# Kernel optimization log

Measured on AMD Instinct MI355X. Metric: run time of the kernel, lower is better.

## Reference

```python
import jax, jax.numpy as jnp
import numpy as np

HQ, HKV = 16, 4          # query heads, kv heads
ROPE_BASE = 10000.0


def _rope(t, positions):
    # t: [B, H, S, hd]; standard rotate-half RoPE over head_dim
    hd = t.shape[-1]
    inv_freq = 1.0 / (ROPE_BASE ** (jnp.arange(0, hd, 2, dtype=jnp.float32) / hd))
    freqs = positions.astype(jnp.float32)[:, None] * inv_freq[None, :]      # [S, hd/2]
    emb = jnp.concatenate([freqs, freqs], axis=-1)                           # [S, hd]
    cos = jnp.cos(emb)[None, None, :, :].astype(t.dtype)
    sin = jnp.sin(emb)[None, None, :, :].astype(t.dtype)
    t1, t2 = t[..., : hd // 2], t[..., hd // 2 :]
    rot = jnp.concatenate([-t2, t1], axis=-1)
    return t * cos + rot * sin


def setup_inputs() -> dict:
    key = jax.random.key(0)
    k0, k1, k2, k3, k4 = jax.random.split(key, 5)
    B, S, D = 2, 2048, 2048
    hd = D // HQ
    x = jax.random.normal(k0, (B, S, D), dtype=jnp.float32)
    s = 0.02
    wq = jax.random.normal(k1, (HQ * hd, D), dtype=jnp.float32) * s
    wk = jax.random.normal(k2, (HKV * hd, D), dtype=jnp.float32) * s
    wv = jax.random.normal(k3, (HKV * hd, D), dtype=jnp.float32) * s
    wo = jax.random.normal(k4, (D, HQ * hd), dtype=jnp.float32) * s
    return {"x": x, "wq": wq, "wk": wk, "wv": wv, "wo": wo}


def reference(x, wq, wk, wv, wo):
    B, S, D = x.shape
    hd = D // HQ
    G = HQ // HKV
    positions = jnp.arange(S)

    q = (x @ wq.T).reshape(B, S, HQ, hd).transpose(0, 2, 1, 3)   # [B,Hq,S,hd]
    k = (x @ wk.T).reshape(B, S, HKV, hd).transpose(0, 2, 1, 3)  # [B,Hkv,S,hd]
    v = (x @ wv.T).reshape(B, S, HKV, hd).transpose(0, 2, 1, 3)

    q = _rope(q, positions)
    k = _rope(k, positions)

    # GQA: expand KV heads to match query heads (repeat_interleave on head dim)
    k = jnp.repeat(k, G, axis=1)
    v = jnp.repeat(v, G, axis=1)

    scores = jnp.einsum("bhqd,bhkd->bhqk", q, k) / jnp.sqrt(jnp.float32(hd))
    causal = jnp.tril(jnp.ones((S, S), dtype=bool))
    scores = jnp.where(causal[None, None], scores, -jnp.inf)
    attn = jax.nn.softmax(scores, axis=-1)

    out = jnp.einsum("bhqk,bhkd->bhqd", attn, v)                 # [B,Hq,S,hd]
    out = out.transpose(0, 2, 1, 3).reshape(B, S, HQ * hd)
    return out @ wo.T
```

## Files before the change

kernel.cpp:

```cpp
#include <hip/hip_runtime.h>

#define B_   2
#define S_   2048
#define D_   2048
#define HQ_  16
#define HKV_ 4
#define HD_  128

typedef __attribute__((ext_vector_type(4))) float f32x4;
typedef __attribute__((ext_vector_type(16))) float f32x16;
typedef __attribute__((ext_vector_type(4))) short s16x4;
typedef __attribute__((ext_vector_type(8))) short s16x8;

static __device__ __forceinline__ ushort f2bf(float f) {
  uint32_t u = __float_as_uint(f);
  u += 0x7fffu + ((u >> 16) & 1u);
  return (ushort)(u >> 16);
}

static __device__ __forceinline__ void gload16(const ushort* g, ushort* l) {
  __builtin_amdgcn_global_load_lds((const __attribute__((address_space(1))) uint32_t*)(g),
                                   (__attribute__((address_space(3))) uint32_t*)(l), 16, 0, 0);
}

__global__ void cast_kernel(const float* __restrict__ in, ushort* __restrict__ out, int n) {
  int i = (blockIdx.x * blockDim.x + threadIdx.x) * 4;
  if (i + 3 < n) {
    float4 v = *(const float4*)(in + i);
    *(ushort4*)(out + i) = make_ushort4(f2bf(v.x), f2bf(v.y), f2bf(v.z), f2bf(v.w));
  }
}

__global__ __launch_bounds__(256) void gemm_nt_bf16(const ushort* __restrict__ A,
                                                    const ushort* __restrict__ Bm,
                                                    float* __restrict__ C,
                                                    int M, int N, int K, int nbx) {
  __shared__ ushort As[128 * 64];
  __shared__ ushort Bs[128 * 64];
  const int nwg = gridDim.x;
  const int per = nwg >> 3;
  const int id = blockIdx.x;
  const int wg = (id & 7) * per + (id >> 3);
  const int bx = wg % nbx, by = wg / nbx;
  const int tid  = threadIdx.x;
  const int lane = tid & 63;
  const int wave = tid >> 6;
  const int lrow = lane & 15, lgrp = lane >> 4;
  const int wm = (wave >> 1) * 64, wn = (wave & 1) * 64;
  const int brow = by * 128, bcol = bx * 128;

  f32x4 acc[4][4];
#pragma unroll
  for (int i = 0; i < 4; ++i)
#pragma unroll
    for (int j = 0; j < 4; ++j) acc[i][j] = (f32x4){0.f, 0.f, 0.f, 0.f};

  const int r_ = tid >> 3, c16 = tid & 7;
  const ushort* Abase = A + (size_t)brow * K;
  const ushort* Bbase = Bm + (size_t)bcol * K;

  for (int k0 = 0; k0 < K; k0 += 64) {
#pragma unroll
    for (int q = 0; q < 4; ++q) {
      const int row = q * 32 + r_;
      const int sc = c16 ^ (row & 7);
      gload16(Abase + (size_t)row * K + k0 + sc * 8, &As[q * 2048 + wave * 512]);
      gload16(Bbase + (size_t)row * K + k0 + sc * 8, &Bs[q * 2048 + wave * 512]);
    }
    __syncthreads();
#pragma unroll
    for (int kc = 0; kc < 2; ++kc) {
      s16x8 aF[4], bF[4];
#pragma unroll
      for (int mt = 0; mt < 4; ++mt) {
        const int row = wm + mt * 16 + lrow;
        aF[mt] = *(const s16x8*)&As[row * 64 + ((kc * 32 + lgrp * 8) ^ ((row & 7) << 3))];
      }
#pragma unroll
      for (int nt = 0; nt < 4; ++nt) {
        const int row = wn + nt * 16 + lrow;
        bF[nt] = *(const s16x8*)&Bs[row * 64 + ((kc * 32 + lgrp * 8) ^ ((row & 7) << 3))];
      }
#pragma unroll
      for (int mt = 0; mt < 4; ++mt)
#pragma unroll
        for (int nt = 0; nt < 4; ++nt)
          acc[mt][nt] = __builtin_amdgcn_mfma_f32_16x16x32_bf16(aF[mt], bF[nt], acc[mt][nt], 0, 0, 0);
    }
    __syncthreads();
  }
#pragma unroll
  for (int mt = 0; mt < 4; ++mt) {
#pragma unroll
    for (int nt = 0; nt < 4; ++nt) {
      const int row = brow + wm + mt * 16 + lgrp * 4;
      const int col = bcol + wn + nt * 16 + lrow;
#pragma unroll
      for (int rr = 0; rr < 4; ++rr)
        C[(size_t)(row + rr) * N + col] = acc[mt][nt][rr];
    }
  }
}

__global__ __launch_bounds__(256) void rope_qk(const float* __restrict__ qkv,
                                               ushort* __restrict__ Qb, ushort* __restrict__ Kb) {
  const int idx = blockIdx.x * 256 + threadIdx.x;
  const int i = idx & 63;
  const int t = idx >> 6;
  const int s = t & (S_ - 1);
  const int b = t >> 11;
  const float inv = exp2f(-(float)i * 0.20762050594046832f);
  float sn, cs;
  sincosf((float)s * inv, &sn, &cs);
  const size_t row = (size_t)t * 3072;
  const float SCL2 = 0.12751744716705736f;
#pragma unroll
  for (int h = 0; h < HQ_; ++h) {
    const float a  = qkv[row + h * 128 + i];
    const float c2 = qkv[row + h * 128 + i + 64];
    const size_t ob = ((size_t)((b * HQ_ + h) * S_ + s)) * 128;
    Qb[ob + i]      = f2bf((a * cs - c2 * sn) * SCL2);
    Qb[ob + i + 64] = f2bf((c2 * cs + a * sn) * SCL2);
  }
#pragma unroll
  for (int kh = 0; kh < HKV_; ++kh) {
    const float a  = qkv[row + 2048 + kh * 128 + i];
    const float c2 = qkv[row + 2048 + kh * 128 + i + 64];
    const size_t ob = ((size_t)((b * HKV_ + kh) * S_ + s)) * 128;
    Kb[ob + i]      = f2bf(a * cs - c2 * sn);
    Kb[ob + i + 64] = f2bf(c2 * cs + a * sn);
  }
}

__global__ __launch_bounds__(256) void v_transpose(const float* __restrict__ qkv, ushort* __restrict__ Vt) {
  __shared__ ushort tile[128][72];
  const int s0 = blockIdx.x * 64;
  const int kh = blockIdx.y;
  const int b  = blockIdx.z;
  for (int idx = threadIdx.x; idx < 64 * 128; idx += 256) {
    int sl = idx >> 7;
    int d  = idx & 127;
    float v = qkv[(size_t)(b * S_ + s0 + sl) * 3072 + 2560 + kh * 128 + d];
    tile[d][sl] = f2bf(v);
  }
  __syncthreads();
  for (int idx = threadIdx.x; idx < 64 * 128; idx += 256) {
    int d  = idx >> 6;
    int sl = idx & 63;
    int sp = (sl & 48) | (sl & 3) | ((sl & 8) >> 1) | ((sl & 4) << 1);
    Vt[((size_t)(b * HKV_ + kh) * 128 + d) * S_ + s0 + sp] = tile[d][sl];
  }
}

__global__ __launch_bounds__(256, 2) void attn_kernel(const ushort* __restrict__ Qb,
                                                      const ushort* __restrict__ Kb,
                                                      const ushort* __restrict__ Vt,
                                                      ushort* __restrict__ Ao) {
  __shared__ ushort Ks[2][64 * 128];
  __shared__ ushort Vs[2][128 * 64];
  const int h = blockIdx.y, b = blockIdx.z, kh = h >> 2;
  const int tid = threadIdx.x, lane = tid & 63, wave = tid >> 6;
  const int lq = lane & 31, g = lane >> 5;
  const ushort* Kg = Kb + ((size_t)(b * HKV_ + kh)) * S_ * HD_;
  const ushort* Vg = Vt + ((size_t)(b * HKV_ + kh)) * HD_ * S_;

  const int qt = b ? (15 - (int)blockIdx.x) : (int)blockIdx.x;
  const int q0 = qt * 128;
  const int qg = q0 + wave * 32 + lq;
  const int nk = 2 * qt + 2;

  s16x8 qF[8];
  {
    const ushort* qrow = Qb + (((size_t)(b * HQ_ + h)) * S_ + qg) * HD_ + g * 8;
#pragma unroll
    for (int s = 0; s < 8; ++s) qF[s] = *(const s16x8*)(qrow + s * 16);
  }

  const char* KsB = (const char*)&Ks[0][0];
  const char* VsB = (const char*)&Vs[0][0];
  uint32_t ka[2], va[4];
#pragma unroll
  for (int t = 0; t < 2; ++t) ka[t] = (uint32_t)(t * 32 + lq) * 256 + ((uint32_t)(g ^ (lq & 15)) << 4);
#pragma unroll
  for (int dt = 0; dt < 4; ++dt) va[dt] = (uint32_t)(dt * 32 + lq) * 128 + ((uint32_t)(g ^ (lq & 7)) << 4);

#define STAGE(buf, kt64)                                                          \
    {                                                                             \
      _Pragma("unroll")                                                           \
      for (int i_ = 0; i_ < 4; ++i_) {                                            \
        const int slot = i_ * 256 + tid;                                          \
        const int r = slot >> 4, c = slot & 15;                                   \
        const int cc = c ^ (r & 15);                                              \
        gload16(Kg + ((size_t)((kt64) * 64 + r)) * HD_ + cc * 8,                  \
                &Ks[buf][i_ * 2048 + wave * 512]);                                \
      }                                                                           \
      _Pragma("unroll")                                                           \
      for (int i_ = 0; i_ < 4; ++i_) {                                            \
        const int slot = i_ * 256 + tid;                                          \
        const int r = slot >> 3, c = slot & 7;                                    \
        const int cc = c ^ (r & 7);                                               \
        gload16(Vg + (size_t)r * S_ + (kt64) * 64 + cc * 8,                       \
                &Vs[buf][i_ * 2048 + wave * 512]);                                \
      }                                                                           \
    }

  f32x16 acc[4] = {};
  float m_run = -3.0e38f, l_run = 0.f;

  STAGE(0, 0);
  asm volatile("s_waitcnt vmcnt(0)" ::: "memory");
  __syncthreads();

#define COMPUTE(CUR, ktv)                                                                   \
  {                                                                                         \
    f32x16 sc[2] = {};                                                                      \
    __builtin_amdgcn_s_setprio(1);                                                          \
    _Pragma("unroll")                                                                       \
    for (int s = 0; s < 8; ++s) {                                                           \
      const s16x8 k0 = *(const s16x8*)(KsB + (ka[0] ^ (uint32_t)(s << 5)) + (CUR)*16384);   \
      const s16x8 k1 = *(const s16x8*)(KsB + (ka[1] ^ (uint32_t)(s << 5)) + (CUR)*16384);   \
      sc[0] = __builtin_amdgcn_mfma_f32_32x32x16_bf16(k0, qF[s], sc[0], 0, 0, 0);           \
      sc[1] = __builtin_amdgcn_mfma_f32_32x32x16_bf16(k1, qF[s], sc[1], 0, 0, 0);           \
    }                                                                                       \
    __builtin_amdgcn_s_setprio(0);                                                          \
    float tmax = -3.0e38f;                                                                  \
    if ((ktv) >= 2 * qt) {                                                                  \
      _Pragma("unroll")                                                                     \
      for (int t = 0; t < 2; ++t)                                                           \
        _Pragma("unroll")                                                                   \
        for (int r = 0; r < 16; ++r) {                                                      \
          const int kg = (ktv) * 64 + t * 32 + (r & 3) + 8 * (r >> 2) + 4 * g;              \
          if (kg > qg) sc[t][r] = -3.0e38f;                                                 \
          tmax = fmaxf(tmax, sc[t][r]);                                                     \
        }                                                                                   \
    } else {                                                                                \
      _Pragma("unroll")                                                                     \
      for (int t = 0; t < 2; ++t)                                                           \
        _Pragma("unroll")                                                                   \
        for (int r = 0; r < 16; ++r) tmax = fmaxf(tmax, sc[t][r]);                          \
    }                                                                                       \
    tmax = fmaxf(tmax, __shfl_xor(tmax, 32, 64));                                           \
    if (!__all(tmax <= m_run + 8.f)) {                                                      \
      const float m_new = fmaxf(m_run, tmax);                                               \
      const float alpha = exp2f(m_run - m_new);                                             \
      m_run = m_new;                                                                        \
      l_run *= alpha;                                                                       \
      _Pragma("unroll")                                                                     \
      for (int dt = 0; dt < 4; ++dt)                                                        \
        _Pragma("unroll")                                                                   \
        for (int r = 0; r < 16; ++r) acc[dt][r] *= alpha;                                   \
    }                                                                                       \
    float psum = 0.f;                                                                       \
    uint32_t pk[16];                                                                        \
    _Pragma("unroll")                                                                       \
    for (int t = 0; t < 2; ++t)                                                             \
      _Pragma("unroll")                                                                     \
      for (int i = 0; i < 8; ++i) {                                                         \
        const float e0 = exp2f(sc[t][2 * i]     - m_run);                                   \
        const float e1 = exp2f(sc[t][2 * i + 1] - m_run);                                   \
        psum += e0 + e1;                                                                    \
        asm("v_cvt_pk_bf16_f32 %0, %1, %2" : "=v"(pk[t * 8 + i]) : "v"(e0), "v"(e1));       \
      }                                                                                     \
    psum += __shfl_xor(psum, 32, 64);                                                       \
    l_run += psum;                                                                          \
    __builtin_amdgcn_s_setprio(1);                                                          \
    _Pragma("unroll")                                                                       \
    for (int ks = 0; ks < 4; ++ks) {                                                        \
      union { s16x8 v; uint32_t u[4]; } pb;                                                 \
      _Pragma("unroll")                                                                     \
      for (int j = 0; j < 4; ++j) pb.u[j] = pk[ks * 4 + j];                                 \
      _Pragma("unroll")                                                                     \
      for (int dt = 0; dt < 4; ++dt) {                                                      \
        const s16x8 vA = *(const s16x8*)(VsB + (va[dt] ^ (uint32_t)(ks << 5)) + (CUR)*16384);\
        acc[dt] = __builtin_amdgcn_mfma_f32_32x32x16_bf16(vA, pb.v, acc[dt], 0, 0, 0);      \
      }                                                                                     \
    }                                                                                       \
    __builtin_amdgcn_s_setprio(0);                                                          \
  }

#pragma unroll 1
  for (int kt = 0; kt < nk; kt += 2) {
    STAGE(1, kt + 1);
    COMPUTE(0, kt);
    asm volatile("s_waitcnt vmcnt(0)" ::: "memory");
    __syncthreads();
    if (kt + 2 < nk) STAGE(0, kt + 2);
    COMPUTE(1, kt + 1);
    asm volatile("s_waitcnt vmcnt(0)" ::: "memory");
    __syncthreads();
  }

  const float inv_l = 1.f / l_run;
  ushort* orow = Ao + ((size_t)(b * S_ + qg)) * D_ + h * HD_;
#pragma unroll
  for (int dt = 0; dt < 4; ++dt)
#pragma unroll
    for (int u = 0; u < 4; ++u) {
      ushort4 w;
      w.x = f2bf(acc[dt][4 * u + 0] * inv_l);
      w.y = f2bf(acc[dt][4 * u + 1] * inv_l);
      w.z = f2bf(acc[dt][4 * u + 2] * inv_l);
      w.w = f2bf(acc[dt][4 * u + 3] * inv_l);
      *(ushort4*)(orow + dt * 32 + 8 * u + 4 * g) = w;
    }
#undef STAGE
#undef COMPUTE
}

extern "C" void kernel_launch(void* const* d_in, const int* in_sizes, int n_in,
                              void* d_out, int out_size, void* d_ws, size_t ws_size,
                              hipStream_t stream) {
  const float* x  = (const float*)d_in[0];
  const float* wq = (const float*)d_in[1];
  const float* wk = (const float*)d_in[2];
  const float* wv = (const float*)d_in[3];
  const float* wo = (const float*)d_in[4];
  float* out = (float*)d_out;
  char* ws = (char*)d_ws;

  ushort* xb    = (ushort*)(ws);
  ushort* wqkvb = (ushort*)(ws + 16777216);
  ushort* wob   = (ushort*)(ws + 29360128);
  float*  qkvf  = (float*) (ws + 37748736);
  ushort* Qb    = (ushort*)(ws + 88080384);
  ushort* Kb    = (ushort*)(ws + 104857600);
  ushort* Vt    = (ushort*)(ws + 109051904);
  ushort* Ao    = (ushort*)(ws + 113246208);

  cast_kernel<<<8192, 256, 0, stream>>>(x,  xb, 8388608);
  cast_kernel<<<4096, 256, 0, stream>>>(wq, wqkvb, 4194304);
  cast_kernel<<<1024, 256, 0, stream>>>(wk, wqkvb + 4194304, 1048576);
  cast_kernel<<<1024, 256, 0, stream>>>(wv, wqkvb + 5242880, 1048576);
  cast_kernel<<<4096, 256, 0, stream>>>(wo, wob, 4194304);

  gemm_nt_bf16<<<768, 256, 0, stream>>>(xb, wqkvb, qkvf, 4096, 3072, 2048, 24);
  rope_qk<<<1024, 256, 0, stream>>>(qkvf, Qb, Kb);
  v_transpose<<<dim3(32, 4, 2), 256, 0, stream>>>(qkvf, Vt);
  attn_kernel<<<dim3(16, 16, 2), 256, 0, stream>>>(Qb, Kb, Vt, Ao);
  gemm_nt_bf16<<<512, 256, 0, stream>>>(Ao, wob, out, 4096, 2048, 2048, 16);
}
```

Measured before the change: 333.0 us.

## Replace GEMM with 256x256 double-buffered pipelined kernel using 8 waves

Swaps the 128x128 single-buffered bf16 GEMM for a 256x256-tile kernel with 512 threads, double-buffered LDS, and staged global->LDS loads interleaved with MFMA phases under s_setprio. The goal is to overlap memory loads with compute and raise data reuse per tile, removing the full-barrier stalls of the old loop. The larger tile cuts grid size to 192 and 128 workgroups, which may leave CUs underfilled on a 256-CU device, and the heavier register and LDS footprint raises occupancy pressure.

```diff
diff --git a/kernel.cpp b/kernel.cpp
--- a/kernel.cpp
+++ b/kernel.cpp
@@ -31,70 +31,159 @@
   }
 }
 
-__global__ __launch_bounds__(256) void gemm_nt_bf16(const ushort* __restrict__ A,
-                                                    const ushort* __restrict__ Bm,
-                                                    float* __restrict__ C,
-                                                    int M, int N, int K, int nbx) {
-  __shared__ ushort As[128 * 64];
-  __shared__ ushort Bs[128 * 64];
+__global__ __launch_bounds__(512, 2) void gemm256(const ushort* __restrict__ A,
+                                                  const ushort* __restrict__ Bm,
+                                                  float* __restrict__ C,
+                                                  int M, int N, int K, int nbx) {
+  __shared__ ushort As[2][16384];
+  __shared__ ushort Bs[2][16384];
   const int nwg = gridDim.x;
   const int per = nwg >> 3;
   const int id = blockIdx.x;
   const int wg = (id & 7) * per + (id >> 3);
   const int bx = wg % nbx, by = wg / nbx;
-  const int tid  = threadIdx.x;
-  const int lane = tid & 63;
-  const int wave = tid >> 6;
+  const int tid = threadIdx.x, lane = tid & 63, wave = tid >> 6;
   const int lrow = lane & 15, lgrp = lane >> 4;
-  const int wm = (wave >> 1) * 64, wn = (wave & 1) * 64;
-  const int brow = by * 128, bcol = bx * 128;
-
-  f32x4 acc[4][4];
-#pragma unroll
-  for (int i = 0; i < 4; ++i)
-#pragma unroll
-    for (int j = 0; j < 4; ++j) acc[i][j] = (f32x4){0.f, 0.f, 0.f, 0.f};
-
-  const int r_ = tid >> 3, c16 = tid & 7;
+  const int wr = wave >> 2, wc = wave & 3;
+  const int brow = by * 256, bcol = bx * 256;
+  const int NT = K >> 6;
+
   const ushort* Abase = A + (size_t)brow * K;
   const ushort* Bbase = Bm + (size_t)bcol * K;
 
-  for (int k0 = 0; k0 < K; k0 += 64) {
-#pragma unroll
-    for (int q = 0; q < 4; ++q) {
-      const int row = q * 32 + r_;
-      const int sc = c16 ^ (row & 7);
-      gload16(Abase + (size_t)row * K + k0 + sc * 8, &As[q * 2048 + wave * 512]);
-      gload16(Bbase + (size_t)row * K + k0 + sc * 8, &Bs[q * 2048 + wave * 512]);
-    }
-    __syncthreads();
-#pragma unroll
-    for (int kc = 0; kc < 2; ++kc) {
-      s16x8 aF[4], bF[4];
-#pragma unroll
-      for (int mt = 0; mt < 4; ++mt) {
-        const int row = wm + mt * 16 + lrow;
-        aF[mt] = *(const s16x8*)&As[row * 64 + ((kc * 32 + lgrp * 8) ^ ((row & 7) << 3))];
-      }
-#pragma unroll
-      for (int nt = 0; nt < 4; ++nt) {
-        const int row = wn + nt * 16 + lrow;
-        bF[nt] = *(const s16x8*)&Bs[row * 64 + ((kc * 32 + lgrp * 8) ^ ((row & 7) << 3))];
-      }
-#pragma unroll
-      for (int mt = 0; mt < 4; ++mt)
-#pragma unroll
-        for (int nt = 0; nt < 4; ++nt)
-          acc[mt][nt] = __builtin_amdgcn_mfma_f32_16x16x32_bf16(aF[mt], bF[nt], acc[mt][nt], 0, 0, 0);
-    }
-    __syncthreads();
-  }
-#pragma unroll
-  for (int mt = 0; mt < 4; ++mt) {
+  f32x4 acc[8][4];
+#pragma unroll
+  for (int i = 0; i < 8; ++i)
+#pragma unroll
+    for (int j = 0; j < 4; ++j) acc[i][j] = (f32x4){0.f, 0.f, 0.f, 0.f};
+
+  s16x8 aF[8][2], bF[4][2];
+
+#define LDA8(BUF, row, kc) (*(const s16x8*)&As[BUF][(row) * 64 + (((kc) * 32 + lgrp * 8) ^ (((row) & 7) << 3))])
+#define LDB8(BUF, row, kc) (*(const s16x8*)&Bs[BUF][(row) * 64 + (((kc) * 32 + lgrp * 8) ^ (((row) & 7) << 3))])
+
+#define STAGE_AH(BUF, H, KT)                                                        \
+  {                                                                                 \
+    _Pragma("unroll")                                                               \
+    for (int i_ = 0; i_ < 2; ++i_) {                                                \
+      const int s_ = i_ * 512 + tid;                                                \
+      const int r_ = s_ >> 3;                                                       \
+      const int cc_ = (s_ & 7) ^ (r_ & 7);                                          \
+      gload16(Abase + (size_t)((H) * 128 + r_) * K + (KT) * 64 + cc_ * 8,           \
+              &As[BUF][(H) * 8192 + i_ * 4096 + wave * 512]);                       \
+    }                                                                               \
+  }
+#define STAGE_BH(BUF, H, KT)                                                        \
+  {                                                                                 \
+    _Pragma("unroll")                                                               \
+    for (int i_ = 0; i_ < 2; ++i_) {                                                \
+      const int s_ = i_ * 512 + tid;                                                \
+      const int r_ = s_ >> 3;                                                       \
+      const int cc_ = (s_ & 7) ^ (r_ & 7);                                          \
+      gload16(Bbase + (size_t)((H) * 128 + r_) * K + (KT) * 64 + cc_ * 8,           \
+              &Bs[BUF][(H) * 8192 + i_ * 4096 + wave * 512]);                       \
+    }                                                                               \
+  }
+
+#define TILE(BUF, J, VMS)                                                           \
+  {                                                                                 \
+    asm volatile("s_waitcnt " VMS ::: "memory");                                    \
+    __builtin_amdgcn_s_barrier();                                                   \
+                                 \
+    _Pragma("unroll")                                                               \
+    for (int mt = 0; mt < 4; ++mt) {                                                \
+      const int row = wr * 128 + mt * 16 + lrow;                                    \
+      aF[mt][0] = LDA8(BUF, row, 0);                                                \
+      aF[mt][1] = LDA8(BUF, row, 1);                                                \
+    }                                                                               \
+    _Pragma("unroll")                                                               \
+    for (int nt = 0; nt < 2; ++nt) {                                                \
+      const int row = wc * 64 + nt * 16 + lrow;                                     \
+      bF[nt][0] = LDB8(BUF, row, 0);                                                \
+      bF[nt][1] = LDB8(BUF, row, 1);                                                \
+    }                                                                               \
+    if ((J) + 1 < NT) STAGE_BH((BUF) ^ 1, 0, (J) + 1);                              \
+    __builtin_amdgcn_s_setprio(1);                                                  \
+    _Pragma("unroll")                                                               \
+    for (int mt = 0; mt < 4; ++mt)                                                  \
+      _Pragma("unroll")                                                             \
+      for (int nt = 0; nt < 2; ++nt) {                                              \
+        acc[mt][nt] = __builtin_amdgcn_mfma_f32_16x16x32_bf16(aF[mt][0], bF[nt][0], acc[mt][nt], 0, 0, 0); \
+        acc[mt][nt] = __builtin_amdgcn_mfma_f32_16x16x32_bf16(aF[mt][1], bF[nt][1], acc[mt][nt], 0, 0, 0); \
+      }                                                                             \
+    __builtin_amdgcn_s_setprio(0);                                                  \
+    __builtin_amdgcn_s_barrier();                                                   \
+                                 \
+    _Pragma("unroll")                                                               \
+    for (int mt = 0; mt < 4; ++mt) {                                                \
+      const int row = wr * 128 + (mt + 4) * 16 + lrow;                              \
+      aF[mt + 4][0] = LDA8(BUF, row, 0);                                            \
+      aF[mt + 4][1] = LDA8(BUF, row, 1);                                            \
+    }                                                                               \
+    _Pragma("unroll")                                                               \
+    for (int nt = 2; nt < 4; ++nt) {                                                \
+      const int row = wc * 64 + nt * 16 + lrow;                                     \
+      bF[nt][0] = LDB8(BUF, row, 0);                                                \
+      bF[nt][1] = LDB8(BUF, row, 1);                                                \
+    }                                                                               \
+    if ((J) + 1 < NT) STAGE_BH((BUF) ^ 1, 1, (J) + 1);                              \
+    __builtin_amdgcn_s_setprio(1);                                                  \
+    _Pragma("unroll")                                                               \
+    for (int mt = 0; mt < 4; ++mt)                                                  \
+      _Pragma("unroll")                                                             \
+      for (int nt = 0; nt < 2; ++nt) {                                              \
+        acc[mt + 4][nt] = __builtin_amdgcn_mfma_f32_16x16x32_bf16(aF[mt + 4][0], bF[nt][0], acc[mt + 4][nt], 0, 0, 0); \
+        acc[mt + 4][nt] = __builtin_amdgcn_mfma_f32_16x16x32_bf16(aF[mt + 4][1], bF[nt][1], acc[mt + 4][nt], 0, 0, 0); \
+      }                                                                             \
+    __builtin_amdgcn_s_setprio(0);                                                  \
+    __builtin_amdgcn_s_barrier();                                                   \
+     \
+    if ((J) + 2 < NT) STAGE_AH(BUF, 0, (J) + 2);                                    \
+    __builtin_amdgcn_s_setprio(1);                                                  \
+    _Pragma("unroll")                                                               \
+    for (int mt = 0; mt < 4; ++mt)                                                  \
+      _Pragma("unroll")                                                             \
+      for (int nt = 2; nt < 4; ++nt) {                                              \
+        acc[mt][nt] = __builtin_amdgcn_mfma_f32_16x16x32_bf16(aF[mt][0], bF[nt][0], acc[mt][nt], 0, 0, 0); \
+        acc[mt][nt] = __builtin_amdgcn_mfma_f32_16x16x32_bf16(aF[mt][1], bF[nt][1], acc[mt][nt], 0, 0, 0); \
+      }                                                                             \
+    __builtin_amdgcn_s_setprio(0);                                                  \
+                                      \
+    if ((J) + 2 < NT) STAGE_AH(BUF, 1, (J) + 2);                                    \
+    __builtin_amdgcn_s_setprio(1);                                                  \
+    _Pragma("unroll")                                                               \
+    for (int mt = 0; mt < 4; ++mt)                                                  \
+      _Pragma("unroll")                                                             \
+      for (int nt = 2; nt < 4; ++nt) {                                              \
+        acc[mt + 4][nt] = __builtin_amdgcn_mfma_f32_16x16x32_bf16(aF[mt + 4][0], bF[nt][0], acc[mt + 4][nt], 0, 0, 0); \
+        acc[mt + 4][nt] = __builtin_amdgcn_mfma_f32_16x16x32_bf16(aF[mt + 4][1], bF[nt][1], acc[mt + 4][nt], 0, 0, 0); \
+      }                                                                             \
+    __builtin_amdgcn_s_setprio(0);                                                  \
+  }
+
+  STAGE_AH(0, 0, 0); STAGE_AH(0, 1, 0); STAGE_BH(0, 0, 0); STAGE_BH(0, 1, 0);
+  STAGE_AH(1, 0, 1); STAGE_AH(1, 1, 1);
+
+#pragma unroll 1
+  for (int j = 0; j < NT - 2; j += 2) {
+    TILE(0, j, "vmcnt(4)");
+    TILE(1, j + 1, "vmcnt(4)");
+  }
+  TILE(0, NT - 2, "vmcnt(4)");
+  TILE(1, NT - 1, "vmcnt(0)");
+
+#undef TILE
+#undef STAGE_AH
+#undef STAGE_BH
+#undef LDA8
+#undef LDB8
+
+#pragma unroll
+  for (int mt = 0; mt < 8; ++mt) {
 #pragma unroll
     for (int nt = 0; nt < 4; ++nt) {
-      const int row = brow + wm + mt * 16 + lgrp * 4;
-      const int col = bcol + wn + nt * 16 + lrow;
+      const int row = brow + wr * 128 + mt * 16 + lgrp * 4;
+      const int col = bcol + wc * 64 + nt * 16 + lrow;
 #pragma unroll
       for (int rr = 0; rr < 4; ++rr)
         C[(size_t)(row + rr) * N + col] = acc[mt][nt][rr];
@@ -333,9 +422,9 @@
   cast_kernel<<<1024, 256, 0, stream>>>(wv, wqkvb + 5242880, 1048576);
   cast_kernel<<<4096, 256, 0, stream>>>(wo, wob, 4194304);
 
-  gemm_nt_bf16<<<768, 256, 0, stream>>>(xb, wqkvb, qkvf, 4096, 3072, 2048, 24);
+  gemm256<<<192, 512, 0, stream>>>(xb, wqkvb, qkvf, 4096, 3072, 2048, 12);
   rope_qk<<<1024, 256, 0, stream>>>(qkvf, Qb, Kb);
   v_transpose<<<dim3(32, 4, 2), 256, 0, stream>>>(qkvf, Vt);
   attn_kernel<<<dim3(16, 16, 2), 256, 0, stream>>>(Qb, Kb, Vt, Ao);
-  gemm_nt_bf16<<<512, 256, 0, stream>>>(Ao, wob, out, 4096, 2048, 2048, 16);
-}
+  gemm256<<<128, 512, 0, stream>>>(Ao, wob, out, 4096, 2048, 2048, 8);
+}
```

Result: slower. 339.7 us (+2.0%).
